# Performance work log

Measured on AMD Instinct MI355X. Metric: run time of the kernel, lower is better.

The kernel has to match this reference:

```python
import jax, jax.numpy as jnp
import numpy as np

HID = 16

def _lrconv(x, edge_index, edge_attr, w1, b1, w2, b2):
    # flow='target_to_source': x_i = x[edge_index[0]], x_j = x[edge_index[1]],
    # aggregate (max) at edge_index[0].
    src = edge_index[0]
    dst = edge_index[1]
    m = jnp.concatenate([x[src], x[dst], edge_attr], axis=-1)  # [E, 2*in+edge]
    m = jax.nn.relu(m @ w1 + b1)
    m = jax.nn.relu(m @ w2 + b2)  # [E, out], all >= 0
    agg = jax.ops.segment_max(m, src, num_segments=x.shape[0])
    # empty segments get -inf in jax; PyG fills with 0. Messages are ReLU'd (>=0),
    # so clamping at 0 is exact.
    return jnp.maximum(agg, 0.0)

def _glorot(key, shape):
    fan_in, fan_out = shape
    lim = float(np.sqrt(6.0 / (fan_in + fan_out)))
    return jax.random.uniform(key, shape, jnp.float32, -lim, lim)

def setup_inputs() -> dict:
    key = jax.random.key(0)
    ks = jax.random.split(key, 16)
    N, E = 100000, 1600000
    x = jax.random.normal(ks[0], (N, 4), jnp.float32)
    edge_index = jax.random.randint(ks[1], (2, E), 0, N, jnp.int64)
    edge_attr = jax.random.normal(ks[2], (E, 8), jnp.float32)
    # conv1: in=4 -> cat dim 4*2+8=16
    c1_w1 = _glorot(ks[3], (16, HID)); c1_b1 = jnp.zeros((HID,), jnp.float32)
    c1_w2 = _glorot(ks[4], (HID, 16)); c1_b2 = jnp.zeros((16,), jnp.float32)
    # conv2: in=16 -> cat dim 16*2+8=40
    c2_w1 = _glorot(ks[5], (40, HID)); c2_b1 = jnp.zeros((HID,), jnp.float32)
    c2_w2 = _glorot(ks[6], (HID, 16)); c2_b2 = jnp.zeros((16,), jnp.float32)
    l1_w = _glorot(ks[7], (16, 16)); l1_b = jnp.zeros((16,), jnp.float32)
    l2_w = _glorot(ks[8], (16, 1)); l2_b = jnp.zeros((1,), jnp.float32)
    return {"x": x, "edge_index": edge_index, "edge_attr": edge_attr,
            "c1_w1": c1_w1, "c1_b1": c1_b1, "c1_w2": c1_w2, "c1_b2": c1_b2,
            "c2_w1": c2_w1, "c2_b1": c2_b1, "c2_w2": c2_w2, "c2_b2": c2_b2,
            "l1_w": l1_w, "l1_b": l1_b, "l2_w": l2_w, "l2_b": l2_b}

def reference(x, edge_index, edge_attr,
              c1_w1, c1_b1, c1_w2, c1_b2,
              c2_w1, c2_b1, c2_w2, c2_b2,
              l1_w, l1_b, l2_w, l2_b):
    h = _lrconv(x, edge_index, edge_attr, c1_w1, c1_b1, c1_w2, c1_b2)   # [N,16]
    h = _lrconv(h, edge_index, edge_attr, c2_w1, c2_b1, c2_w2, c2_b2)   # [N,16]
    h = jax.nn.relu(h @ l1_w + l1_b)
    return h @ l2_w + l2_b  # [N,1]
```

## Files before the change

### kernel.cpp

```cpp
#include <hip/hip_runtime.h>
#include <hip/hip_fp16.h>

#define CHUNK 1024
#define NBKT 4

typedef _Float16 half8 __attribute__((ext_vector_type(8)));
typedef float floatx4 __attribute__((ext_vector_type(4)));

__device__ __forceinline__ unsigned int pack2(float a, float b) {
    __half2 h = __floats2half2_rn(a, b);
    return *(unsigned int*)&h;
}
__device__ __forceinline__ float2 unpack2(unsigned int u) {
    __half2 h = *(__half2*)&u;
    return __half22float2(h);
}

__global__ __launch_bounds__(256) void rank_cvt(
    const int* __restrict__ ei, const float* __restrict__ ea,
    int* __restrict__ deg, unsigned short* __restrict__ r,
    _Float16* __restrict__ eah, int E)
{
    int e = blockIdx.x * 256 + threadIdx.x;
    if (e >= E) return;
    int bkt = (e >> 8) & (NBKT - 1);
    r[e] = (unsigned short)atomicAdd(&deg[(size_t)ei[e] * NBKT + bkt], 1);
    float4 a0 = *(const float4*)(ea + (size_t)e * 8);
    float4 a1 = *(const float4*)(ea + (size_t)e * 8 + 4);
    half8 h;
    h[0] = (_Float16)a0.x; h[1] = (_Float16)a0.y;
    h[2] = (_Float16)a0.z; h[3] = (_Float16)a0.w;
    h[4] = (_Float16)a1.x; h[5] = (_Float16)a1.y;
    h[6] = (_Float16)a1.z; h[7] = (_Float16)a1.w;
    *(half8*)(eah + (size_t)e * 8) = h;
}

__global__ __launch_bounds__(256) void scan_chunk_sums(
    const int* __restrict__ v, int* __restrict__ csum, int N)
{
    __shared__ int s[256];
    int base = blockIdx.x * CHUNK;
    int t = threadIdx.x;
    int acc = 0;
    #pragma unroll
    for (int i = 0; i < CHUNK / 256; ++i) {
        int idx = base + t + i * 256;
        if (idx < N) acc += v[idx];
    }
    s[t] = acc; __syncthreads();
    for (int o = 128; o > 0; o >>= 1) {
        if (t < o) s[t] += s[t + o];
        __syncthreads();
    }
    if (t == 0) csum[blockIdx.x] = s[0];
}

__global__ __launch_bounds__(256) void scan_chunk_off(
    const int* __restrict__ csum, int* __restrict__ coff, int nch)
{
    __shared__ int s[256];
    __shared__ int carry;
    int t = threadIdx.x;
    if (t == 0) carry = 0;
    __syncthreads();
    for (int base = 0; base < nch; base += 256) {
        int v = (base + t < nch) ? csum[base + t] : 0;
        s[t] = v; __syncthreads();
        for (int o = 1; o < 256; o <<= 1) {
            int add = (t >= o) ? s[t - o] : 0;
            __syncthreads();
            s[t] += add;
            __syncthreads();
        }
        int excl = carry + (t > 0 ? s[t - 1] : 0);
        if (base + t < nch) coff[base + t] = excl;
        __syncthreads();
        if (t == 0) carry += s[255];
        __syncthreads();
    }
}

__global__ __launch_bounds__(256) void scan_within_excl(
    const int* __restrict__ deg, int* __restrict__ pos,
    const int* __restrict__ coff, int N)
{
    __shared__ int s[256];
    int t = threadIdx.x;
    int base = blockIdx.x * CHUNK + t * 4;
    int v0 = 0, v1 = 0, v2 = 0, v3 = 0;
    if (base + 0 < N) v0 = deg[base + 0];
    if (base + 1 < N) v1 = deg[base + 1];
    if (base + 2 < N) v2 = deg[base + 2];
    if (base + 3 < N) v3 = deg[base + 3];
    s[t] = v0 + v1 + v2 + v3;
    __syncthreads();
    for (int o = 1; o < 256; o <<= 1) {
        int add = (t >= o) ? s[t - o] : 0;
        __syncthreads();
        s[t] += add;
        __syncthreads();
    }
    int run = coff[blockIdx.x] + (t > 0 ? s[t - 1] : 0);
    if (base + 0 < N) pos[base + 0] = run; run += v0;
    if (base + 1 < N) pos[base + 1] = run; run += v1;
    if (base + 2 < N) pos[base + 2] = run; run += v2;
    if (base + 3 < N) pos[base + 3] = run;
}

__global__ __launch_bounds__(256) void edge_mlp1(
    const float* __restrict__ x,
    const int*   __restrict__ ei,
    const _Float16* __restrict__ eah,
    const int*   __restrict__ pos,
    const unsigned short* __restrict__ r,
    const float* __restrict__ w1, const float* __restrict__ b1,
    const float* __restrict__ w2, const float* __restrict__ b2,
    _Float16* __restrict__ m2h,
    int E)
{
    __shared__ _Float16 itm[4][4][16][24];
    int tid = threadIdx.x;
    int w = tid >> 6, lane = tid & 63;
    int e16 = lane & 15, q = lane >> 4;
    int ntiles = (E + 63) >> 6;
    int tile = blockIdx.x * 4 + w;
    if (tile >= ntiles) return;
    int ebase = tile << 6;
    int e = ebase + lane;

    int s_l = 0, d_l = 0, p_l = 0;
    if (e < E) {
        s_l = ei[e];
        d_l = ei[E + e];
        p_l = pos[(size_t)s_l * NBKT + ((e >> 8) & (NBKT - 1))] + (int)r[e];
    }

    half8 B1, B2;
    #pragma unroll
    for (int j = 0; j < 8; ++j) { B1[j] = (_Float16)0.f; B2[j] = (_Float16)0.f; }
    if (q < 2) {
        #pragma unroll
        for (int j = 0; j < 8; ++j) {
            B1[j] = (_Float16)w1[(8 * q + j) * 16 + e16];
            B2[j] = (_Float16)w2[(8 * q + j) * 16 + e16];
        }
    }
    float b1c = b1[e16], b2c = b2[e16];

    half8 A[4];
    #pragma unroll
    for (int t = 0; t < 4; ++t) {
        int st = __shfl(s_l, 16 * t + e16, 64);
        int dt = __shfl(d_l, 16 * t + e16, 64);
        half8 a;
        #pragma unroll
        for (int j = 0; j < 8; ++j) a[j] = (_Float16)0.f;
        int et = ebase + 16 * t + e16;
        if (q == 0 && et < E) {
            float4 xs = *(const float4*)(x + (size_t)st * 4);
            float4 xd = *(const float4*)(x + (size_t)dt * 4);
            a[0] = (_Float16)xs.x; a[1] = (_Float16)xs.y;
            a[2] = (_Float16)xs.z; a[3] = (_Float16)xs.w;
            a[4] = (_Float16)xd.x; a[5] = (_Float16)xd.y;
            a[6] = (_Float16)xd.z; a[7] = (_Float16)xd.w;
        } else if (q == 1 && et < E) {
            a = *(const half8*)(eah + (size_t)et * 8);
        }
        A[t] = a;
    }

    floatx4 C[4];
    #pragma unroll
    for (int t = 0; t < 4; ++t) {
        floatx4 c = {b1c, b1c, b1c, b1c};
        C[t] = __builtin_amdgcn_mfma_f32_16x16x32_f16(A[t], B1, c, 0, 0, 0);
    }
    #pragma unroll
    for (int t = 0; t < 4; ++t)
        #pragma unroll
        for (int i = 0; i < 4; ++i)
            itm[w][t][4 * q + i][e16] = (_Float16)fmaxf(C[t][i], 0.0f);
    __builtin_amdgcn_wave_barrier();

    half8 A2[4];
    #pragma unroll
    for (int t = 0; t < 4; ++t) {
        half8 a;
        #pragma unroll
        for (int j = 0; j < 8; ++j) a[j] = (_Float16)0.f;
        if (q < 2) a = *(const half8*)&itm[w][t][e16][8 * q];
        A2[t] = a;
    }
    __builtin_amdgcn_wave_barrier();
    floatx4 C2[4];
    #pragma unroll
    for (int t = 0; t < 4; ++t) {
        floatx4 c = {b2c, b2c, b2c, b2c};
        C2[t] = __builtin_amdgcn_mfma_f32_16x16x32_f16(A2[t], B2, c, 0, 0, 0);
    }
    #pragma unroll
    for (int t = 0; t < 4; ++t)
        #pragma unroll
        for (int i = 0; i < 4; ++i)
            itm[w][t][4 * q + i][e16] = (_Float16)C2[t][i];
    __builtin_amdgcn_wave_barrier();

    if (e < E) {
        half8 lo = *(const half8*)&itm[w][q][e16][0];
        half8 hi = *(const half8*)&itm[w][q][e16][8];
        *(half8*)(m2h + (size_t)p_l * 16)     = lo;
        *(half8*)(m2h + (size_t)p_l * 16 + 8) = hi;
    }
}

__global__ __launch_bounds__(256) void edge_mlp2(
    const float* __restrict__ hw_s,
    const unsigned short* __restrict__ hw_dh,
    const int*   __restrict__ ei,
    const _Float16* __restrict__ eah,
    const int*   __restrict__ pos,
    const unsigned short* __restrict__ r,
    const float* __restrict__ w1,
    const float* __restrict__ w2, const float* __restrict__ b2,
    _Float16* __restrict__ m2h, int E)
{
    __shared__ _Float16 itm[4][4][16][24];
    int tid = threadIdx.x;
    int w = tid >> 6, lane = tid & 63;
    int e16 = lane & 15, q = lane >> 4;
    const __half* hwd = (const __half*)hw_dh;
    int ntiles = (E + 63) >> 6;
    int tile = blockIdx.x * 4 + w;
    if (tile >= ntiles) return;
    int ebase = tile << 6;
    int e = ebase + lane;

    int s_l = 0, d_l = 0, p_l = 0;
    if (e < E) {
        s_l = ei[e];
        d_l = ei[E + e];
        p_l = pos[(size_t)s_l * NBKT + ((e >> 8) & (NBKT - 1))] + (int)r[e];
    }

    half8 B1, B2;
    #pragma unroll
    for (int j = 0; j < 8; ++j) { B1[j] = (_Float16)0.f; B2[j] = (_Float16)0.f; }
    if (q == 0) {
        #pragma unroll
        for (int j = 0; j < 8; ++j)
            B1[j] = (_Float16)w1[(32 + j) * 16 + e16];
    }
    if (q < 2) {
        #pragma unroll
        for (int j = 0; j < 8; ++j)
            B2[j] = (_Float16)w2[(8 * q + j) * 16 + e16];
    }
    float b2c = b2[e16];

    half8 A[4];
    #pragma unroll
    for (int t = 0; t < 4; ++t) {
        half8 a;
        #pragma unroll
        for (int j = 0; j < 8; ++j) a[j] = (_Float16)0.f;
        int et = ebase + 16 * t + e16;
        if (q == 0 && et < E)
            a = *(const half8*)(eah + (size_t)et * 8);
        A[t] = a;
    }

    floatx4 C[4];
    #pragma unroll
    for (int t = 0; t < 4; ++t) {
        floatx4 c;
        #pragma unroll
        for (int i = 0; i < 4; ++i) {
            int li = 16 * t + 4 * q + i;
            int s = __shfl(s_l, li, 64);
            int d = __shfl(d_l, li, 64);
            int rr = ebase + li;
            float v = 0.0f;
            if (rr < E) {
                v = hw_s[(size_t)s * 16 + e16]
                  + __half2float(hwd[(size_t)d * 16 + e16]);
            }
            c[i] = v;
        }
        C[t] = __builtin_amdgcn_mfma_f32_16x16x32_f16(A[t], B1, c, 0, 0, 0);
    }
    #pragma unroll
    for (int t = 0; t < 4; ++t)
        #pragma unroll
        for (int i = 0; i < 4; ++i)
            itm[w][t][4 * q + i][e16] = (_Float16)fmaxf(C[t][i], 0.0f);
    __builtin_amdgcn_wave_barrier();

    half8 A2[4];
    #pragma unroll
    for (int t = 0; t < 4; ++t) {
        half8 a;
        #pragma unroll
        for (int j = 0; j < 8; ++j) a[j] = (_Float16)0.f;
        if (q < 2) a = *(const half8*)&itm[w][t][e16][8 * q];
        A2[t] = a;
    }
    __builtin_amdgcn_wave_barrier();
    floatx4 C2[4];
    #pragma unroll
    for (int t = 0; t < 4; ++t) {
        floatx4 c = {b2c, b2c, b2c, b2c};
        C2[t] = __builtin_amdgcn_mfma_f32_16x16x32_f16(A2[t], B2, c, 0, 0, 0);
    }
    #pragma unroll
    for (int t = 0; t < 4; ++t)
        #pragma unroll
        for (int i = 0; i < 4; ++i)
            itm[w][t][4 * q + i][e16] = (_Float16)C2[t][i];
    __builtin_amdgcn_wave_barrier();

    if (e < E) {
        half8 lo = *(const half8*)&itm[w][q][e16][0];
        half8 hi = *(const half8*)&itm[w][q][e16][8];
        *(half8*)(m2h + (size_t)p_l * 16)     = lo;
        *(half8*)(m2h + (size_t)p_l * 16 + 8) = hi;
    }
}

__global__ __launch_bounds__(256) void segmax1_hw(
    const _Float16* __restrict__ m2h, const int* __restrict__ pos,
    const float* __restrict__ cw1, const float* __restrict__ cb1,
    float* __restrict__ hw_s, unsigned short* __restrict__ hw_dh,
    int N, int E)
{
    int tid = threadIdx.x;
    int n = blockIdx.x * 32 + (tid >> 3);
    if (n >= N) return;
    int g = tid & 7;
    int start = pos[(size_t)n * NBKT];
    int end = (n + 1 < N) ? pos[(size_t)(n + 1) * NBKT] : E;

    float acc[16];
    #pragma unroll
    for (int j = 0; j < 16; ++j) acc[j] = 0.0f;

    for (int k = start + g; k < end; k += 8) {
        uint4 u0 = *(const uint4*)(m2h + (size_t)k * 16);
        uint4 u1 = *(const uint4*)(m2h + (size_t)k * 16 + 8);
        float2 f;
        f = unpack2(u0.x); acc[0]  = fmaxf(acc[0],  f.x); acc[1]  = fmaxf(acc[1],  f.y);
        f = unpack2(u0.y); acc[2]  = fmaxf(acc[2],  f.x); acc[3]  = fmaxf(acc[3],  f.y);
        f = unpack2(u0.z); acc[4]  = fmaxf(acc[4],  f.x); acc[5]  = fmaxf(acc[5],  f.y);
        f = unpack2(u0.w); acc[6]  = fmaxf(acc[6],  f.x); acc[7]  = fmaxf(acc[7],  f.y);
        f = unpack2(u1.x); acc[8]  = fmaxf(acc[8],  f.x); acc[9]  = fmaxf(acc[9],  f.y);
        f = unpack2(u1.y); acc[10] = fmaxf(acc[10], f.x); acc[11] = fmaxf(acc[11], f.y);
        f = unpack2(u1.z); acc[12] = fmaxf(acc[12], f.x); acc[13] = fmaxf(acc[13], f.y);
        f = unpack2(u1.w); acc[14] = fmaxf(acc[14], f.x); acc[15] = fmaxf(acc[15], f.y);
    }
    #pragma unroll
    for (int mask = 1; mask < 8; mask <<= 1) {
        #pragma unroll
        for (int j = 0; j < 16; ++j)
            acc[j] = fmaxf(acc[j], __shfl_xor(acc[j], mask, 64));
    }

    int j0 = 2 * g, j1 = 2 * g + 1;
    float hs0 = cb1[j0], hs1 = cb1[j1], hd0 = 0.0f, hd1 = 0.0f;
    #pragma unroll
    for (int k = 0; k < 16; ++k) {
        float ak = acc[k];
        hs0 = fmaf(ak, cw1[k * 16 + j0], hs0);
        hs1 = fmaf(ak, cw1[k * 16 + j1], hs1);
        hd0 = fmaf(ak, cw1[(16 + k) * 16 + j0], hd0);
        hd1 = fmaf(ak, cw1[(16 + k) * 16 + j1], hd1);
    }
    *(float2*)(hw_s + (size_t)n * 16 + j0) = make_float2(hs0, hs1);
    ((unsigned int*)hw_dh)[(size_t)n * 8 + g] = pack2(hd0, hd1);
}

__global__ __launch_bounds__(256) void segmax2_head(
    const _Float16* __restrict__ m2h, const int* __restrict__ pos,
    const float* __restrict__ l1w, const float* __restrict__ l1b,
    const float* __restrict__ l2w, const float* __restrict__ l2b,
    float* __restrict__ out, int N, int E)
{
    int tid = threadIdx.x;
    int n = blockIdx.x * 32 + (tid >> 3);
    if (n >= N) return;
    int g = tid & 7;
    int start = pos[(size_t)n * NBKT];
    int end = (n + 1 < N) ? pos[(size_t)(n + 1) * NBKT] : E;

    float acc[16];
    #pragma unroll
    for (int j = 0; j < 16; ++j) acc[j] = 0.0f;

    for (int k = start + g; k < end; k += 8) {
        uint4 u0 = *(const uint4*)(m2h + (size_t)k * 16);
        uint4 u1 = *(const uint4*)(m2h + (size_t)k * 16 + 8);
        float2 f;
        f = unpack2(u0.x); acc[0]  = fmaxf(acc[0],  f.x); acc[1]  = fmaxf(acc[1],  f.y);
        f = unpack2(u0.y); acc[2]  = fmaxf(acc[2],  f.x); acc[3]  = fmaxf(acc[3],  f.y);
        f = unpack2(u0.z); acc[4]  = fmaxf(acc[4],  f.x); acc[5]  = fmaxf(acc[5],  f.y);
        f = unpack2(u0.w); acc[6]  = fmaxf(acc[6],  f.x); acc[7]  = fmaxf(acc[7],  f.y);
        f = unpack2(u1.x); acc[8]  = fmaxf(acc[8],  f.x); acc[9]  = fmaxf(acc[9],  f.y);
        f = unpack2(u1.y); acc[10] = fmaxf(acc[10], f.x); acc[11] = fmaxf(acc[11], f.y);
        f = unpack2(u1.z); acc[12] = fmaxf(acc[12], f.x); acc[13] = fmaxf(acc[13], f.y);
        f = unpack2(u1.w); acc[14] = fmaxf(acc[14], f.x); acc[15] = fmaxf(acc[15], f.y);
    }
    #pragma unroll
    for (int mask = 1; mask < 8; mask <<= 1) {
        #pragma unroll
        for (int j = 0; j < 16; ++j)
            acc[j] = fmaxf(acc[j], __shfl_xor(acc[j], mask, 64));
    }

    float t2[16];
    #pragma unroll
    for (int j = 0; j < 16; ++j) t2[j] = l1b[j];
    #pragma unroll
    for (int kk = 0; kk < 16; ++kk) {
        float ak = acc[kk];
        #pragma unroll
        for (int j = 0; j < 16; ++j) t2[j] = fmaf(ak, l1w[kk * 16 + j], t2[j]);
    }
    float r2 = l2b[0];
    #pragma unroll
    for (int j = 0; j < 16; ++j) r2 = fmaf(fmaxf(t2[j], 0.0f), l2w[j], r2);
    if (g == 0) out[n] = r2;
}

extern "C" void kernel_launch(void* const* d_in, const int* in_sizes, int n_in,
                              void* d_out, int out_size, void* d_ws, size_t ws_size,
                              hipStream_t stream)
{
    const float* x     = (const float*)d_in[0];
    const int*   ei    = (const int*)  d_in[1];
    const float* ea    = (const float*)d_in[2];
    const float* c1_w1 = (const float*)d_in[3];
    const float* c1_b1 = (const float*)d_in[4];
    const float* c1_w2 = (const float*)d_in[5];
    const float* c1_b2 = (const float*)d_in[6];
    const float* c2_w1 = (const float*)d_in[7];
    const float* c2_b1 = (const float*)d_in[8];
    const float* c2_w2 = (const float*)d_in[9];
    const float* c2_b2 = (const float*)d_in[10];
    const float* l1_w  = (const float*)d_in[11];
    const float* l1_b  = (const float*)d_in[12];
    const float* l2_w  = (const float*)d_in[13];
    const float* l2_b  = (const float*)d_in[14];
    float* out = (float*)d_out;

    const int N = in_sizes[0] / 4;
    const int E = in_sizes[2] / 8;
    const int M = N * NBKT;
    const int nch = (M + CHUNK - 1) / CHUNK;

    const int BLK = 256;
    const int egrid = (E + BLK - 1) / BLK;
    const int ggrid = (N + 31) / 32;
    const int ntiles64 = (E + 63) >> 6;
    const int mgrid = (ntiles64 + 3) / 4;

    size_t szN16f = (size_t)N * 16 * 4;
    size_t szN16h = (size_t)N * 16 * 2;
    size_t szPos  = ((size_t)M * 4 + 15) & ~(size_t)15;
    size_t szEh   = ((size_t)E * 2 + 15) & ~(size_t)15;
    size_t szE16  = (size_t)E * 16;

    size_t pos_off  = 0;
    size_t r_off    = pos_off  + szPos;
    size_t hws_off  = r_off    + szEh;
    size_t hwdh_off = hws_off  + szN16f;
    size_t eah_off  = hwdh_off + szN16h;
    size_t m2h_off  = eah_off  + szE16;
    size_t deg_off  = m2h_off;
    size_t cs_off   = deg_off  + szPos;
    size_t cf_off   = cs_off   + 16384;

    int*            pos  = (int*)  ((char*)d_ws + pos_off);
    unsigned short* r    = (unsigned short*)((char*)d_ws + r_off);
    float*          hw_s = (float*)((char*)d_ws + hws_off);
    unsigned short* hwdh = (unsigned short*)((char*)d_ws + hwdh_off);
    _Float16*       eah  = (_Float16*)((char*)d_ws + eah_off);
    _Float16*       m2h  = (_Float16*)((char*)d_ws + m2h_off);
    int*            deg  = (int*)  ((char*)d_ws + deg_off);
    int*            csum = (int*)  ((char*)d_ws + cs_off);
    int*            coff = (int*)  ((char*)d_ws + cf_off);

    hipMemsetAsync(deg, 0, (size_t)M * 4, stream);
    rank_cvt<<<egrid, BLK, 0, stream>>>(ei, ea, deg, r, eah, E);
    scan_chunk_sums<<<nch, BLK, 0, stream>>>(deg, csum, M);
    scan_chunk_off<<<1, 256, 0, stream>>>(csum, coff, nch);
    scan_within_excl<<<nch, BLK, 0, stream>>>(deg, pos, coff, M);
    edge_mlp1<<<mgrid, BLK, 0, stream>>>(x, ei, eah, pos, r,
                                         c1_w1, c1_b1, c1_w2, c1_b2, m2h, E);
    segmax1_hw<<<ggrid, BLK, 0, stream>>>(m2h, pos, c2_w1, c2_b1,
                                          hw_s, hwdh, N, E);
    edge_mlp2<<<mgrid, BLK, 0, stream>>>(hw_s, hwdh, ei, eah, pos, r,
                                         c2_w1, c2_w2, c2_b2, m2h, E);
    segmax2_head<<<ggrid, BLK, 0, stream>>>(m2h, pos, l1_w, l1_b, l2_w, l2_b,
                                            out, N, E);
}
```

Measured before the change: 363.1 us.

## Sort edges by source once and fuse segment-max into edge MLP kernels

Adds a CSR scatter pass that stores each edge's (src,dst) and half-precision edge attributes in source-sorted order. Both edge-MLP kernels then read edges contiguously and reduce messages into a shared-memory per-node max buffer, flushing it to a global float aggregate with atomicMax. Blocks whose node span is too wide fall back to global atomics. This drops the E×16 message buffer writes and the separate segment-max read passes. The cost is extra memsets, the scatter pass and atomic contention; the bucket count is also raised from 4 to 8.

```diff
diff --git a/kernel.cpp b/kernel.cpp
--- a/kernel.cpp
+++ b/kernel.cpp
@@ -2,7 +2,8 @@
 #include <hip/hip_fp16.h>
 
 #define CHUNK 1024
-#define NBKT 4
+#define NBKT 8
+#define SPAN 128
 
 typedef _Float16 half8 __attribute__((ext_vector_type(8)));
 typedef float floatx4 __attribute__((ext_vector_type(4)));
@@ -11,28 +12,15 @@
     __half2 h = __floats2half2_rn(a, b);
     return *(unsigned int*)&h;
 }
-__device__ __forceinline__ float2 unpack2(unsigned int u) {
-    __half2 h = *(__half2*)&u;
-    return __half22float2(h);
-}
 
 __global__ __launch_bounds__(256) void rank_cvt(
-    const int* __restrict__ ei, const float* __restrict__ ea,
-    int* __restrict__ deg, unsigned short* __restrict__ r,
-    _Float16* __restrict__ eah, int E)
+    const int* __restrict__ ei, int* __restrict__ deg,
+    unsigned short* __restrict__ r, int E)
 {
     int e = blockIdx.x * 256 + threadIdx.x;
     if (e >= E) return;
     int bkt = (e >> 8) & (NBKT - 1);
     r[e] = (unsigned short)atomicAdd(&deg[(size_t)ei[e] * NBKT + bkt], 1);
-    float4 a0 = *(const float4*)(ea + (size_t)e * 8);
-    float4 a1 = *(const float4*)(ea + (size_t)e * 8 + 4);
-    half8 h;
-    h[0] = (_Float16)a0.x; h[1] = (_Float16)a0.y;
-    h[2] = (_Float16)a0.z; h[3] = (_Float16)a0.w;
-    h[4] = (_Float16)a1.x; h[5] = (_Float16)a1.y;
-    h[6] = (_Float16)a1.z; h[7] = (_Float16)a1.w;
-    *(half8*)(eah + (size_t)e * 8) = h;
 }
 
 __global__ __launch_bounds__(256) void scan_chunk_sums(
@@ -107,33 +95,62 @@
     if (base + 3 < N) pos[base + 3] = run;
 }
 
-__global__ __launch_bounds__(256) void edge_mlp1(
+__global__ __launch_bounds__(256) void csr_scatter(
+    const int* __restrict__ ei, const float* __restrict__ ea,
+    const int* __restrict__ pos, const unsigned short* __restrict__ r,
+    int2* __restrict__ sd, _Float16* __restrict__ eahc, int E)
+{
+    int e = blockIdx.x * 256 + threadIdx.x;
+    if (e >= E) return;
+    int s = ei[e];
+    int d = ei[E + e];
+    int p = pos[(size_t)s * NBKT + ((e >> 8) & (NBKT - 1))] + (int)r[e];
+    float4 a0 = *(const float4*)(ea + (size_t)e * 8);
+    float4 a1 = *(const float4*)(ea + (size_t)e * 8 + 4);
+    half8 h;
+    h[0] = (_Float16)a0.x; h[1] = (_Float16)a0.y;
+    h[2] = (_Float16)a0.z; h[3] = (_Float16)a0.w;
+    h[4] = (_Float16)a1.x; h[5] = (_Float16)a1.y;
+    h[6] = (_Float16)a1.z; h[7] = (_Float16)a1.w;
+    sd[p] = make_int2(s, d);
+    *(half8*)(eahc + (size_t)p * 8) = h;
+}
+
+__global__ __launch_bounds__(256) void edge_mlp1_agg(
     const float* __restrict__ x,
-    const int*   __restrict__ ei,
-    const _Float16* __restrict__ eah,
-    const int*   __restrict__ pos,
-    const unsigned short* __restrict__ r,
+    const int2*  __restrict__ sd,
+    const _Float16* __restrict__ eahc,
     const float* __restrict__ w1, const float* __restrict__ b1,
     const float* __restrict__ w2, const float* __restrict__ b2,
-    _Float16* __restrict__ m2h,
+    float* __restrict__ agg,
     int E)
 {
     __shared__ _Float16 itm[4][4][16][24];
+    __shared__ int lmax[SPAN * 16];
     int tid = threadIdx.x;
     int w = tid >> 6, lane = tid & 63;
     int e16 = lane & 15, q = lane >> 4;
-    int ntiles = (E + 63) >> 6;
-    int tile = blockIdx.x * 4 + w;
-    if (tile >= ntiles) return;
-    int ebase = tile << 6;
+    int kbase = blockIdx.x * 256;
+    int ebase = kbase + (w << 6);
     int e = ebase + lane;
-
-    int s_l = 0, d_l = 0, p_l = 0;
-    if (e < E) {
-        s_l = ei[e];
-        d_l = ei[E + e];
-        p_l = pos[(size_t)s_l * NBKT + ((e >> 8) & (NBKT - 1))] + (int)r[e];
-    }
+    bool bvalid = kbase < E;
+
+    #pragma unroll
+    for (int i = 0; i < SPAN * 16 / 256; ++i) lmax[tid + i * 256] = 0;
+
+    int n_first = 0, span = 0;
+    bool fb = false;
+    if (bvalid) {
+        int klast = min(kbase + 255, E - 1);
+        n_first = sd[kbase].x;
+        int n_last = sd[klast].x;
+        span = n_last - n_first + 1;
+        fb = (span > SPAN);
+    }
+    __syncthreads();
+
+    int s_l = 0, d_l = 0;
+    if (e < E) { int2 p = sd[e]; s_l = p.x; d_l = p.y; }
 
     half8 B1, B2;
     #pragma unroll
@@ -164,7 +181,7 @@
             a[4] = (_Float16)xd.x; a[5] = (_Float16)xd.y;
             a[6] = (_Float16)xd.z; a[7] = (_Float16)xd.w;
         } else if (q == 1 && et < E) {
-            a = *(const half8*)(eah + (size_t)et * 8);
+            a = *(const half8*)(eahc + (size_t)et * 8);
         }
         A[t] = a;
     }
@@ -198,49 +215,69 @@
         floatx4 c = {b2c, b2c, b2c, b2c};
         C2[t] = __builtin_amdgcn_mfma_f32_16x16x32_f16(A2[t], B2, c, 0, 0, 0);
     }
-    #pragma unroll
-    for (int t = 0; t < 4; ++t)
-        #pragma unroll
-        for (int i = 0; i < 4; ++i)
-            itm[w][t][4 * q + i][e16] = (_Float16)C2[t][i];
-    __builtin_amdgcn_wave_barrier();
-
-    if (e < E) {
-        half8 lo = *(const half8*)&itm[w][q][e16][0];
-        half8 hi = *(const half8*)&itm[w][q][e16][8];
-        *(half8*)(m2h + (size_t)p_l * 16)     = lo;
-        *(half8*)(m2h + (size_t)p_l * 16 + 8) = hi;
-    }
-}
-
-__global__ __launch_bounds__(256) void edge_mlp2(
+
+    int* agg_i = (int*)agg;
+    #pragma unroll
+    for (int t = 0; t < 4; ++t) {
+        #pragma unroll
+        for (int i = 0; i < 4; ++i) {
+            int li = 16 * t + 4 * q + i;
+            int nn = __shfl(s_l, li, 64);
+            int et = ebase + li;
+            if (et < E) {
+                int bits = __float_as_int(fmaxf(C2[t][i], 0.0f));
+                if (!fb) atomicMax(&lmax[(nn - n_first) * 16 + e16], bits);
+                else     atomicMax(&agg_i[(size_t)nn * 16 + e16], bits);
+            }
+        }
+    }
+    __syncthreads();
+    if (bvalid && !fb) {
+        int tot = span * 16;
+        for (int idx = tid; idx < tot; idx += 256) {
+            int v = lmax[idx];
+            if (v != 0)
+                atomicMax(&agg_i[(size_t)(n_first + (idx >> 4)) * 16 + (idx & 15)], v);
+        }
+    }
+}
+
+__global__ __launch_bounds__(256) void edge_mlp2_agg(
     const float* __restrict__ hw_s,
     const unsigned short* __restrict__ hw_dh,
-    const int*   __restrict__ ei,
-    const _Float16* __restrict__ eah,
-    const int*   __restrict__ pos,
-    const unsigned short* __restrict__ r,
+    const int2*  __restrict__ sd,
+    const _Float16* __restrict__ eahc,
     const float* __restrict__ w1,
     const float* __restrict__ w2, const float* __restrict__ b2,
-    _Float16* __restrict__ m2h, int E)
+    float* __restrict__ agg, int E)
 {
     __shared__ _Float16 itm[4][4][16][24];
+    __shared__ int lmax[SPAN * 16];
     int tid = threadIdx.x;
     int w = tid >> 6, lane = tid & 63;
     int e16 = lane & 15, q = lane >> 4;
     const __half* hwd = (const __half*)hw_dh;
-    int ntiles = (E + 63) >> 6;
-    int tile = blockIdx.x * 4 + w;
-    if (tile >= ntiles) return;
-    int ebase = tile << 6;
+    int kbase = blockIdx.x * 256;
+    int ebase = kbase + (w << 6);
     int e = ebase + lane;
-
-    int s_l = 0, d_l = 0, p_l = 0;
-    if (e < E) {
-        s_l = ei[e];
-        d_l = ei[E + e];
-        p_l = pos[(size_t)s_l * NBKT + ((e >> 8) & (NBKT - 1))] + (int)r[e];
-    }
+    bool bvalid = kbase < E;
+
+    #pragma unroll
+    for (int i = 0; i < SPAN * 16 / 256; ++i) lmax[tid + i * 256] = 0;
+
+    int n_first = 0, span = 0;
+    bool fb = false;
+    if (bvalid) {
+        int klast = min(kbase + 255, E - 1);
+        n_first = sd[kbase].x;
+        int n_last = sd[klast].x;
+        span = n_last - n_first + 1;
+        fb = (span > SPAN);
+    }
+    __syncthreads();
+
+    int s_l = 0, d_l = 0;
+    if (e < E) { int2 p = sd[e]; s_l = p.x; d_l = p.y; }
 
     half8 B1, B2;
     #pragma unroll
@@ -265,10 +302,11 @@
         for (int j = 0; j < 8; ++j) a[j] = (_Float16)0.f;
         int et = ebase + 16 * t + e16;
         if (q == 0 && et < E)
-            a = *(const half8*)(eah + (size_t)et * 8);
+            a = *(const half8*)(eahc + (size_t)et * 8);
         A[t] = a;
     }
 
+    int sv[4][4];
     floatx4 C[4];
     #pragma unroll
     for (int t = 0; t < 4; ++t) {
@@ -278,6 +316,7 @@
             int li = 16 * t + 4 * q + i;
             int s = __shfl(s_l, li, 64);
             int d = __shfl(d_l, li, 64);
+            sv[t][i] = s;
             int rr = ebase + li;
             float v = 0.0f;
             if (rr < E) {
@@ -311,58 +350,46 @@
         floatx4 c = {b2c, b2c, b2c, b2c};
         C2[t] = __builtin_amdgcn_mfma_f32_16x16x32_f16(A2[t], B2, c, 0, 0, 0);
     }
-    #pragma unroll
-    for (int t = 0; t < 4; ++t)
-        #pragma unroll
-        for (int i = 0; i < 4; ++i)
-            itm[w][t][4 * q + i][e16] = (_Float16)C2[t][i];
-    __builtin_amdgcn_wave_barrier();
-
-    if (e < E) {
-        half8 lo = *(const half8*)&itm[w][q][e16][0];
-        half8 hi = *(const half8*)&itm[w][q][e16][8];
-        *(half8*)(m2h + (size_t)p_l * 16)     = lo;
-        *(half8*)(m2h + (size_t)p_l * 16 + 8) = hi;
-    }
-}
-
-__global__ __launch_bounds__(256) void segmax1_hw(
-    const _Float16* __restrict__ m2h, const int* __restrict__ pos,
+
+    int* agg_i = (int*)agg;
+    #pragma unroll
+    for (int t = 0; t < 4; ++t) {
+        #pragma unroll
+        for (int i = 0; i < 4; ++i) {
+            int li = 16 * t + 4 * q + i;
+            int et = ebase + li;
+            if (et < E) {
+                int nn = sv[t][i];
+                int bits = __float_as_int(fmaxf(C2[t][i], 0.0f));
+                if (!fb) atomicMax(&lmax[(nn - n_first) * 16 + e16], bits);
+                else     atomicMax(&agg_i[(size_t)nn * 16 + e16], bits);
+            }
+        }
+    }
+    __syncthreads();
+    if (bvalid && !fb) {
+        int tot = span * 16;
+        for (int idx = tid; idx < tot; idx += 256) {
+            int v = lmax[idx];
+            if (v != 0)
+                atomicMax(&agg_i[(size_t)(n_first + (idx >> 4)) * 16 + (idx & 15)], v);
+        }
+    }
+}
+
+__global__ __launch_bounds__(256) void hw_compute(
+    const float* __restrict__ agg,
     const float* __restrict__ cw1, const float* __restrict__ cb1,
-    float* __restrict__ hw_s, unsigned short* __restrict__ hw_dh,
-    int N, int E)
+    float* __restrict__ hw_s, unsigned short* __restrict__ hw_dh, int N)
 {
     int tid = threadIdx.x;
     int n = blockIdx.x * 32 + (tid >> 3);
     if (n >= N) return;
     int g = tid & 7;
-    int start = pos[(size_t)n * NBKT];
-    int end = (n + 1 < N) ? pos[(size_t)(n + 1) * NBKT] : E;
-
-    float acc[16];
-    #pragma unroll
-    for (int j = 0; j < 16; ++j) acc[j] = 0.0f;
-
-    for (int k = start + g; k < end; k += 8) {
-        uint4 u0 = *(const uint4*)(m2h + (size_t)k * 16);
-        uint4 u1 = *(const uint4*)(m2h + (size_t)k * 16 + 8);
-        float2 f;
-        f = unpack2(u0.x); acc[0]  = fmaxf(acc[0],  f.x); acc[1]  = fmaxf(acc[1],  f.y);
-        f = unpack2(u0.y); acc[2]  = fmaxf(acc[2],  f.x); acc[3]  = fmaxf(acc[3],  f.y);
-        f = unpack2(u0.z); acc[4]  = fmaxf(acc[4],  f.x); acc[5]  = fmaxf(acc[5],  f.y);
-        f = unpack2(u0.w); acc[6]  = fmaxf(acc[6],  f.x); acc[7]  = fmaxf(acc[7],  f.y);
-        f = unpack2(u1.x); acc[8]  = fmaxf(acc[8],  f.x); acc[9]  = fmaxf(acc[9],  f.y);
-        f = unpack2(u1.y); acc[10] = fmaxf(acc[10], f.x); acc[11] = fmaxf(acc[11], f.y);
-        f = unpack2(u1.z); acc[12] = fmaxf(acc[12], f.x); acc[13] = fmaxf(acc[13], f.y);
-        f = unpack2(u1.w); acc[14] = fmaxf(acc[14], f.x); acc[15] = fmaxf(acc[15], f.y);
-    }
-    #pragma unroll
-    for (int mask = 1; mask < 8; mask <<= 1) {
-        #pragma unroll
-        for (int j = 0; j < 16; ++j)
-            acc[j] = fmaxf(acc[j], __shfl_xor(acc[j], mask, 64));
-    }
-
+    const float4* ar = (const float4*)(agg + (size_t)n * 16);
+    float4 A0 = ar[0], A1 = ar[1], A2 = ar[2], A3 = ar[3];
+    float acc[16] = {A0.x, A0.y, A0.z, A0.w, A1.x, A1.y, A1.z, A1.w,
+                     A2.x, A2.y, A2.z, A2.w, A3.x, A3.y, A3.z, A3.w};
     int j0 = 2 * g, j1 = 2 * g + 1;
     float hs0 = cb1[j0], hs1 = cb1[j1], hd0 = 0.0f, hd1 = 0.0f;
     #pragma unroll
@@ -377,56 +404,31 @@
     ((unsigned int*)hw_dh)[(size_t)n * 8 + g] = pack2(hd0, hd1);
 }
 
-__global__ __launch_bounds__(256) void segmax2_head(
-    const _Float16* __restrict__ m2h, const int* __restrict__ pos,
+__global__ __launch_bounds__(256) void head_out(
+    const float* __restrict__ agg,
     const float* __restrict__ l1w, const float* __restrict__ l1b,
     const float* __restrict__ l2w, const float* __restrict__ l2b,
-    float* __restrict__ out, int N, int E)
-{
-    int tid = threadIdx.x;
-    int n = blockIdx.x * 32 + (tid >> 3);
+    float* __restrict__ out, int N)
+{
+    int n = blockIdx.x * 256 + threadIdx.x;
     if (n >= N) return;
-    int g = tid & 7;
-    int start = pos[(size_t)n * NBKT];
-    int end = (n + 1 < N) ? pos[(size_t)(n + 1) * NBKT] : E;
-
-    float acc[16];
-    #pragma unroll
-    for (int j = 0; j < 16; ++j) acc[j] = 0.0f;
-
-    for (int k = start + g; k < end; k += 8) {
-        uint4 u0 = *(const uint4*)(m2h + (size_t)k * 16);
-        uint4 u1 = *(const uint4*)(m2h + (size_t)k * 16 + 8);
-        float2 f;
-        f = unpack2(u0.x); acc[0]  = fmaxf(acc[0],  f.x); acc[1]  = fmaxf(acc[1],  f.y);
-        f = unpack2(u0.y); acc[2]  = fmaxf(acc[2],  f.x); acc[3]  = fmaxf(acc[3],  f.y);
-        f = unpack2(u0.z); acc[4]  = fmaxf(acc[4],  f.x); acc[5]  = fmaxf(acc[5],  f.y);
-        f = unpack2(u0.w); acc[6]  = fmaxf(acc[6],  f.x); acc[7]  = fmaxf(acc[7],  f.y);
-        f = unpack2(u1.x); acc[8]  = fmaxf(acc[8],  f.x); acc[9]  = fmaxf(acc[9],  f.y);
-        f = unpack2(u1.y); acc[10] = fmaxf(acc[10], f.x); acc[11] = fmaxf(acc[11], f.y);
-        f = unpack2(u1.z); acc[12] = fmaxf(acc[12], f.x); acc[13] = fmaxf(acc[13], f.y);
-        f = unpack2(u1.w); acc[14] = fmaxf(acc[14], f.x); acc[15] = fmaxf(acc[15], f.y);
-    }
-    #pragma unroll
-    for (int mask = 1; mask < 8; mask <<= 1) {
-        #pragma unroll
-        for (int j = 0; j < 16; ++j)
-            acc[j] = fmaxf(acc[j], __shfl_xor(acc[j], mask, 64));
-    }
-
+    const float4* ar = (const float4*)(agg + (size_t)n * 16);
+    float4 A0 = ar[0], A1 = ar[1], A2 = ar[2], A3 = ar[3];
+    float acc[16] = {A0.x, A0.y, A0.z, A0.w, A1.x, A1.y, A1.z, A1.w,
+                     A2.x, A2.y, A2.z, A2.w, A3.x, A3.y, A3.z, A3.w};
     float t2[16];
     #pragma unroll
     for (int j = 0; j < 16; ++j) t2[j] = l1b[j];
     #pragma unroll
-    for (int kk = 0; kk < 16; ++kk) {
-        float ak = acc[kk];
-        #pragma unroll
-        for (int j = 0; j < 16; ++j) t2[j] = fmaf(ak, l1w[kk * 16 + j], t2[j]);
+    for (int k = 0; k < 16; ++k) {
+        float ak = acc[k];
+        #pragma unroll
+        for (int j = 0; j < 16; ++j) t2[j] = fmaf(ak, l1w[k * 16 + j], t2[j]);
     }
     float r2 = l2b[0];
     #pragma unroll
     for (int j = 0; j < 16; ++j) r2 = fmaf(fmaxf(t2[j], 0.0f), l2w[j], r2);
-    if (g == 0) out[n] = r2;
+    out[n] = r2;
 }
 
 extern "C" void kernel_launch(void* const* d_in, const int* in_sizes, int n_in,
@@ -458,46 +460,52 @@
     const int BLK = 256;
     const int egrid = (E + BLK - 1) / BLK;
     const int ggrid = (N + 31) / 32;
-    const int ntiles64 = (E + 63) >> 6;
-    const int mgrid = (ntiles64 + 3) / 4;
-
-    size_t szN16f = (size_t)N * 16 * 4;
-    size_t szN16h = (size_t)N * 16 * 2;
+    const int ngrid = (N + 255) / 256;
+    const int mgrid = (E + 255) / 256;
+
     size_t szPos  = ((size_t)M * 4 + 15) & ~(size_t)15;
     size_t szEh   = ((size_t)E * 2 + 15) & ~(size_t)15;
-    size_t szE16  = (size_t)E * 16;
+    size_t szSd   = (size_t)E * 8;
+    size_t szEah  = (size_t)E * 16;
+    size_t szAgg  = (size_t)N * 16 * 4;
+    size_t szHws  = (size_t)N * 16 * 4;
+    size_t szHwd  = (size_t)N * 16 * 2;
 
     size_t pos_off  = 0;
     size_t r_off    = pos_off  + szPos;
-    size_t hws_off  = r_off    + szEh;
-    size_t hwdh_off = hws_off  + szN16f;
-    size_t eah_off  = hwdh_off + szN16h;
-    size_t m2h_off  = eah_off  + szE16;
-    size_t deg_off  = m2h_off;
+    size_t sd_off   = r_off    + szEh;
+    size_t eah_off  = sd_off   + szSd;
+    size_t agg_off  = eah_off  + szEah;
+    size_t hws_off  = agg_off  + szAgg;
+    size_t hwdh_off = hws_off  + szHws;
+    size_t deg_off  = agg_off;
     size_t cs_off   = deg_off  + szPos;
     size_t cf_off   = cs_off   + 16384;
 
     int*            pos  = (int*)  ((char*)d_ws + pos_off);
     unsigned short* r    = (unsigned short*)((char*)d_ws + r_off);
+    int2*           sd   = (int2*) ((char*)d_ws + sd_off);
+    _Float16*       eahc = (_Float16*)((char*)d_ws + eah_off);
+    float*          agg  = (float*)((char*)d_ws + agg_off);
     float*          hw_s = (float*)((char*)d_ws + hws_off);
     unsigned short* hwdh = (unsigned short*)((char*)d_ws + hwdh_off);
-    _Float16*       eah  = (_Float16*)((char*)d_ws + eah_off);
-    _Float16*       m2h  = (_Float16*)((char*)d_ws + m2h_off);
     int*            deg  = (int*)  ((char*)d_ws + deg_off);
     int*            csum = (int*)  ((char*)d_ws + cs_off);
     int*            coff = (int*)  ((char*)d_ws + cf_off);
 
     hipMemsetAsync(deg, 0, (size_t)M * 4, stream);
-    rank_cvt<<<egrid, BLK, 0, stream>>>(ei, ea, deg, r, eah, E);
+    rank_cvt<<<egrid, BLK, 0, stream>>>(ei, deg, r, E);
     scan_chunk_sums<<<nch, BLK, 0, stream>>>(deg, csum, M);
     scan_chunk_off<<<1, 256, 0, stream>>>(csum, coff, nch);
     scan_within_excl<<<nch, BLK, 0, stream>>>(deg, pos, coff, M);
-    edge_mlp1<<<mgrid, BLK, 0, stream>>>(x, ei, eah, pos, r,
-                                         c1_w1, c1_b1, c1_w2, c1_b2, m2h, E);
-    segmax1_hw<<<ggrid, BLK, 0, stream>>>(m2h, pos, c2_w1, c2_b1,
-                                          hw_s, hwdh, N, E);
-    edge_mlp2<<<mgrid, BLK, 0, stream>>>(hw_s, hwdh, ei, eah, pos, r,
-                                         c2_w1, c2_w2, c2_b2, m2h, E);
-    segmax2_head<<<ggrid, BLK, 0, stream>>>(m2h, pos, l1_w, l1_b, l2_w, l2_b,
-                                            out, N, E);
-}
+    hipMemsetAsync(agg, 0, szAgg, stream);
+    csr_scatter<<<egrid, BLK, 0, stream>>>(ei, ea, pos, r, sd, eahc, E);
+    edge_mlp1_agg<<<mgrid, BLK, 0, stream>>>(x, sd, eahc,
+                                             c1_w1, c1_b1, c1_w2, c1_b2,
+                                             agg, E);
+    hw_compute<<<ggrid, BLK, 0, stream>>>(agg, c2_w1, c2_b1, hw_s, hwdh, N);
+    hipMemsetAsync(agg, 0, szAgg, stream);
+    edge_mlp2_agg<<<mgrid, BLK, 0, stream>>>(hw_s, hwdh, sd, eahc,
+                                             c2_w1, c2_w2, c2_b2, agg, E);
+    head_out<<<ngrid, BLK, 0, stream>>>(agg, l1_w, l1_b, l2_w, l2_b, out, N);
+}
```

New measurement: 384.0 us. +5.8%, slower.

## Write edge messages in edge order and gather through sorted edge-id index

Applied to the files above, without the earlier changes.

The fused rank/fp16-conversion pass becomes a plain degree count. Each edge's position is now claimed with an atomic cursor inside edge_mlp1, which records the edge id in a sorted index instead of scattering the message. Both edge MLPs write messages contiguously by edge id and read fp32 edge attributes directly, so the precomputed fp16 copy and the rank array are gone. The segment-max kernels now follow eid indirection, turning contiguous reads into random 32-byte gathers. The bucket count per node rises from 4 to 8 to spread atomic contention.

```diff
diff --git a/kernel.cpp b/kernel.cpp
--- a/kernel.cpp
+++ b/kernel.cpp
@@ -2,7 +2,7 @@
 #include <hip/hip_fp16.h>
 
 #define CHUNK 1024
-#define NBKT 4
+#define NBKT 8
 
 typedef _Float16 half8 __attribute__((ext_vector_type(8)));
 typedef float floatx4 __attribute__((ext_vector_type(4)));
@@ -16,23 +16,12 @@
     return __half22float2(h);
 }
 
-__global__ __launch_bounds__(256) void rank_cvt(
-    const int* __restrict__ ei, const float* __restrict__ ea,
-    int* __restrict__ deg, unsigned short* __restrict__ r,
-    _Float16* __restrict__ eah, int E)
+__global__ __launch_bounds__(256) void count_deg(
+    const int* __restrict__ ei, int* __restrict__ deg, int E)
 {
     int e = blockIdx.x * 256 + threadIdx.x;
     if (e >= E) return;
-    int bkt = (e >> 8) & (NBKT - 1);
-    r[e] = (unsigned short)atomicAdd(&deg[(size_t)ei[e] * NBKT + bkt], 1);
-    float4 a0 = *(const float4*)(ea + (size_t)e * 8);
-    float4 a1 = *(const float4*)(ea + (size_t)e * 8 + 4);
-    half8 h;
-    h[0] = (_Float16)a0.x; h[1] = (_Float16)a0.y;
-    h[2] = (_Float16)a0.z; h[3] = (_Float16)a0.w;
-    h[4] = (_Float16)a1.x; h[5] = (_Float16)a1.y;
-    h[6] = (_Float16)a1.z; h[7] = (_Float16)a1.w;
-    *(half8*)(eah + (size_t)e * 8) = h;
+    atomicAdd(&deg[(size_t)ei[e] * NBKT + ((e >> 8) & (NBKT - 1))], 1);
 }
 
 __global__ __launch_bounds__(256) void scan_chunk_sums(
@@ -110,9 +99,9 @@
 __global__ __launch_bounds__(256) void edge_mlp1(
     const float* __restrict__ x,
     const int*   __restrict__ ei,
-    const _Float16* __restrict__ eah,
-    const int*   __restrict__ pos,
-    const unsigned short* __restrict__ r,
+    const float* __restrict__ ea,
+    int*         __restrict__ cursor,
+    int*         __restrict__ eid,
     const float* __restrict__ w1, const float* __restrict__ b1,
     const float* __restrict__ w2, const float* __restrict__ b2,
     _Float16* __restrict__ m2h,
@@ -122,17 +111,14 @@
     int tid = threadIdx.x;
     int w = tid >> 6, lane = tid & 63;
     int e16 = lane & 15, q = lane >> 4;
-    int ntiles = (E + 63) >> 6;
-    int tile = blockIdx.x * 4 + w;
-    if (tile >= ntiles) return;
-    int ebase = tile << 6;
+    int ebase = (blockIdx.x * 4 + w) << 6;
     int e = ebase + lane;
 
     int s_l = 0, d_l = 0, p_l = 0;
     if (e < E) {
         s_l = ei[e];
         d_l = ei[E + e];
-        p_l = pos[(size_t)s_l * NBKT + ((e >> 8) & (NBKT - 1))] + (int)r[e];
+        p_l = atomicAdd(&cursor[(size_t)s_l * NBKT + ((e >> 8) & (NBKT - 1))], 1);
     }
 
     half8 B1, B2;
@@ -164,7 +150,12 @@
             a[4] = (_Float16)xd.x; a[5] = (_Float16)xd.y;
             a[6] = (_Float16)xd.z; a[7] = (_Float16)xd.w;
         } else if (q == 1 && et < E) {
-            a = *(const half8*)(eah + (size_t)et * 8);
+            float4 a0 = *(const float4*)(ea + (size_t)et * 8);
+            float4 a1 = *(const float4*)(ea + (size_t)et * 8 + 4);
+            a[0] = (_Float16)a0.x; a[1] = (_Float16)a0.y;
+            a[2] = (_Float16)a0.z; a[3] = (_Float16)a0.w;
+            a[4] = (_Float16)a1.x; a[5] = (_Float16)a1.y;
+            a[6] = (_Float16)a1.z; a[7] = (_Float16)a1.w;
         }
         A[t] = a;
     }
@@ -208,8 +199,9 @@
     if (e < E) {
         half8 lo = *(const half8*)&itm[w][q][e16][0];
         half8 hi = *(const half8*)&itm[w][q][e16][8];
-        *(half8*)(m2h + (size_t)p_l * 16)     = lo;
-        *(half8*)(m2h + (size_t)p_l * 16 + 8) = hi;
+        *(half8*)(m2h + (size_t)e * 16)     = lo;
+        *(half8*)(m2h + (size_t)e * 16 + 8) = hi;
+        eid[p_l] = e;
     }
 }
 
@@ -217,9 +209,7 @@
     const float* __restrict__ hw_s,
     const unsigned short* __restrict__ hw_dh,
     const int*   __restrict__ ei,
-    const _Float16* __restrict__ eah,
-    const int*   __restrict__ pos,
-    const unsigned short* __restrict__ r,
+    const float* __restrict__ ea,
     const float* __restrict__ w1,
     const float* __restrict__ w2, const float* __restrict__ b2,
     _Float16* __restrict__ m2h, int E)
@@ -229,17 +219,13 @@
     int w = tid >> 6, lane = tid & 63;
     int e16 = lane & 15, q = lane >> 4;
     const __half* hwd = (const __half*)hw_dh;
-    int ntiles = (E + 63) >> 6;
-    int tile = blockIdx.x * 4 + w;
-    if (tile >= ntiles) return;
-    int ebase = tile << 6;
+    int ebase = (blockIdx.x * 4 + w) << 6;
     int e = ebase + lane;
 
-    int s_l = 0, d_l = 0, p_l = 0;
+    int s_l = 0, d_l = 0;
     if (e < E) {
         s_l = ei[e];
         d_l = ei[E + e];
-        p_l = pos[(size_t)s_l * NBKT + ((e >> 8) & (NBKT - 1))] + (int)r[e];
     }
 
     half8 B1, B2;
@@ -264,8 +250,14 @@
         #pragma unroll
         for (int j = 0; j < 8; ++j) a[j] = (_Float16)0.f;
         int et = ebase + 16 * t + e16;
-        if (q == 0 && et < E)
-            a = *(const half8*)(eah + (size_t)et * 8);
+        if (q == 0 && et < E) {
+            float4 a0 = *(const float4*)(ea + (size_t)et * 8);
+            float4 a1 = *(const float4*)(ea + (size_t)et * 8 + 4);
+            a[0] = (_Float16)a0.x; a[1] = (_Float16)a0.y;
+            a[2] = (_Float16)a0.z; a[3] = (_Float16)a0.w;
+            a[4] = (_Float16)a1.x; a[5] = (_Float16)a1.y;
+            a[6] = (_Float16)a1.z; a[7] = (_Float16)a1.w;
+        }
         A[t] = a;
     }
 
@@ -321,13 +313,14 @@
     if (e < E) {
         half8 lo = *(const half8*)&itm[w][q][e16][0];
         half8 hi = *(const half8*)&itm[w][q][e16][8];
-        *(half8*)(m2h + (size_t)p_l * 16)     = lo;
-        *(half8*)(m2h + (size_t)p_l * 16 + 8) = hi;
+        *(half8*)(m2h + (size_t)e * 16)     = lo;
+        *(half8*)(m2h + (size_t)e * 16 + 8) = hi;
     }
 }
 
 __global__ __launch_bounds__(256) void segmax1_hw(
-    const _Float16* __restrict__ m2h, const int* __restrict__ pos,
+    const _Float16* __restrict__ m2h, const int* __restrict__ eid,
+    const int* __restrict__ cur,
     const float* __restrict__ cw1, const float* __restrict__ cb1,
     float* __restrict__ hw_s, unsigned short* __restrict__ hw_dh,
     int N, int E)
@@ -336,16 +329,17 @@
     int n = blockIdx.x * 32 + (tid >> 3);
     if (n >= N) return;
     int g = tid & 7;
-    int start = pos[(size_t)n * NBKT];
-    int end = (n + 1 < N) ? pos[(size_t)(n + 1) * NBKT] : E;
+    int start = (n == 0) ? 0 : cur[(size_t)n * NBKT - 1];
+    int end = cur[(size_t)(n + 1) * NBKT - 1];
 
     float acc[16];
     #pragma unroll
     for (int j = 0; j < 16; ++j) acc[j] = 0.0f;
 
     for (int k = start + g; k < end; k += 8) {
-        uint4 u0 = *(const uint4*)(m2h + (size_t)k * 16);
-        uint4 u1 = *(const uint4*)(m2h + (size_t)k * 16 + 8);
+        int idx = eid[k];
+        uint4 u0 = *(const uint4*)(m2h + (size_t)idx * 16);
+        uint4 u1 = *(const uint4*)(m2h + (size_t)idx * 16 + 8);
         float2 f;
         f = unpack2(u0.x); acc[0]  = fmaxf(acc[0],  f.x); acc[1]  = fmaxf(acc[1],  f.y);
         f = unpack2(u0.y); acc[2]  = fmaxf(acc[2],  f.x); acc[3]  = fmaxf(acc[3],  f.y);
@@ -378,7 +372,8 @@
 }
 
 __global__ __launch_bounds__(256) void segmax2_head(
-    const _Float16* __restrict__ m2h, const int* __restrict__ pos,
+    const _Float16* __restrict__ m2h, const int* __restrict__ eid,
+    const int* __restrict__ cur,
     const float* __restrict__ l1w, const float* __restrict__ l1b,
     const float* __restrict__ l2w, const float* __restrict__ l2b,
     float* __restrict__ out, int N, int E)
@@ -387,16 +382,17 @@
     int n = blockIdx.x * 32 + (tid >> 3);
     if (n >= N) return;
     int g = tid & 7;
-    int start = pos[(size_t)n * NBKT];
-    int end = (n + 1 < N) ? pos[(size_t)(n + 1) * NBKT] : E;
+    int start = (n == 0) ? 0 : cur[(size_t)n * NBKT - 1];
+    int end = cur[(size_t)(n + 1) * NBKT - 1];
 
     float acc[16];
     #pragma unroll
     for (int j = 0; j < 16; ++j) acc[j] = 0.0f;
 
     for (int k = start + g; k < end; k += 8) {
-        uint4 u0 = *(const uint4*)(m2h + (size_t)k * 16);
-        uint4 u1 = *(const uint4*)(m2h + (size_t)k * 16 + 8);
+        int idx = eid[k];
+        uint4 u0 = *(const uint4*)(m2h + (size_t)idx * 16);
+        uint4 u1 = *(const uint4*)(m2h + (size_t)idx * 16 + 8);
         float2 f;
         f = unpack2(u0.x); acc[0]  = fmaxf(acc[0],  f.x); acc[1]  = fmaxf(acc[1],  f.y);
         f = unpack2(u0.y); acc[2]  = fmaxf(acc[2],  f.x); acc[3]  = fmaxf(acc[3],  f.y);
@@ -461,43 +457,41 @@
     const int ntiles64 = (E + 63) >> 6;
     const int mgrid = (ntiles64 + 3) / 4;
 
-    size_t szN16f = (size_t)N * 16 * 4;
-    size_t szN16h = (size_t)N * 16 * 2;
-    size_t szPos  = ((size_t)M * 4 + 15) & ~(size_t)15;
-    size_t szEh   = ((size_t)E * 2 + 15) & ~(size_t)15;
-    size_t szE16  = (size_t)E * 16;
-
-    size_t pos_off  = 0;
-    size_t r_off    = pos_off  + szPos;
-    size_t hws_off  = r_off    + szEh;
-    size_t hwdh_off = hws_off  + szN16f;
-    size_t eah_off  = hwdh_off + szN16h;
-    size_t m2h_off  = eah_off  + szE16;
+    size_t szEid = ((size_t)E * 4 + 15) & ~(size_t)15;
+    size_t szM2h = (size_t)E * 32;
+    size_t szHws = (size_t)N * 16 * 4;
+    size_t szHwd = (size_t)N * 16 * 2;
+    size_t szCur = ((size_t)M * 4 + 15) & ~(size_t)15;
+
+    size_t eid_off  = 0;
+    size_t m2h_off  = eid_off  + szEid;
+    size_t hws_off  = m2h_off  + szM2h;
+    size_t hwdh_off = hws_off  + szHws;
+    size_t cur_off  = hwdh_off + szHwd;
     size_t deg_off  = m2h_off;
-    size_t cs_off   = deg_off  + szPos;
-    size_t cf_off   = cs_off   + 16384;
-
-    int*            pos  = (int*)  ((char*)d_ws + pos_off);
-    unsigned short* r    = (unsigned short*)((char*)d_ws + r_off);
+    size_t cs_off   = deg_off + szCur;
+    size_t cf_off   = cs_off + 16384;
+
+    int*            eid  = (int*)  ((char*)d_ws + eid_off);
+    _Float16*       m2h  = (_Float16*)((char*)d_ws + m2h_off);
     float*          hw_s = (float*)((char*)d_ws + hws_off);
     unsigned short* hwdh = (unsigned short*)((char*)d_ws + hwdh_off);
-    _Float16*       eah  = (_Float16*)((char*)d_ws + eah_off);
-    _Float16*       m2h  = (_Float16*)((char*)d_ws + m2h_off);
+    int*            cur  = (int*)  ((char*)d_ws + cur_off);
     int*            deg  = (int*)  ((char*)d_ws + deg_off);
     int*            csum = (int*)  ((char*)d_ws + cs_off);
     int*            coff = (int*)  ((char*)d_ws + cf_off);
 
     hipMemsetAsync(deg, 0, (size_t)M * 4, stream);
-    rank_cvt<<<egrid, BLK, 0, stream>>>(ei, ea, deg, r, eah, E);
+    count_deg<<<egrid, BLK, 0, stream>>>(ei, deg, E);
     scan_chunk_sums<<<nch, BLK, 0, stream>>>(deg, csum, M);
     scan_chunk_off<<<1, 256, 0, stream>>>(csum, coff, nch);
-    scan_within_excl<<<nch, BLK, 0, stream>>>(deg, pos, coff, M);
-    edge_mlp1<<<mgrid, BLK, 0, stream>>>(x, ei, eah, pos, r,
+    scan_within_excl<<<nch, BLK, 0, stream>>>(deg, cur, coff, M);
+    edge_mlp1<<<mgrid, BLK, 0, stream>>>(x, ei, ea, cur, eid,
                                          c1_w1, c1_b1, c1_w2, c1_b2, m2h, E);
-    segmax1_hw<<<ggrid, BLK, 0, stream>>>(m2h, pos, c2_w1, c2_b1,
+    segmax1_hw<<<ggrid, BLK, 0, stream>>>(m2h, eid, cur, c2_w1, c2_b1,
                                           hw_s, hwdh, N, E);
-    edge_mlp2<<<mgrid, BLK, 0, stream>>>(hw_s, hwdh, ei, eah, pos, r,
+    edge_mlp2<<<mgrid, BLK, 0, stream>>>(hw_s, hwdh, ei, ea,
                                          c2_w1, c2_w2, c2_b2, m2h, E);
-    segmax2_head<<<ggrid, BLK, 0, stream>>>(m2h, pos, l1_w, l1_b, l2_w, l2_b,
-                                            out, N, E);
-}
+    segmax2_head<<<ggrid, BLK, 0, stream>>>(m2h, eid, cur, l1_w, l1_b,
+                                            l2_w, l2_b, out, N, E);
+}
```

After: 434.7 us. 1.2x slower.
